# Kernel optimization log

Measured on AMD Instinct MI355X. Metric: run time of the kernel, lower is better.

## Reference

```python
import jax, jax.numpy as jnp
import numpy as np

N_FEAT = 6
EMBED = 256
PAIRS = N_FEAT * (N_FEAT - 1) // 2  # 15
B, S = 32, 512


def setup_inputs() -> dict:
    key = jax.random.key(0)
    k1, k2, k3, k4, k5, k6 = jax.random.split(key, 6)
    features = jax.random.normal(k1, (N_FEAT, B, S, EMBED), dtype=jnp.float32)
    W_pair = jax.random.normal(k2, (PAIRS, 2 * EMBED, EMBED), dtype=jnp.float32) * 0.05
    b_pair = jax.random.normal(k3, (PAIRS, EMBED), dtype=jnp.float32) * 0.05
    W_final = jax.random.normal(k4, (PAIRS * EMBED, EMBED), dtype=jnp.float32) * 0.02
    b_final = jax.random.normal(k5, (EMBED,), dtype=jnp.float32) * 0.02
    NAS = jax.random.randint(k6, (N_FEAT,), 0, 2, dtype=jnp.int32)
    return {"features": features, "W_pair": W_pair, "b_pair": b_pair,
            "W_final": W_final, "b_final": b_final, "NAS": NAS}


def reference(features, W_pair, b_pair, W_final, b_final, NAS):
    n = features.shape[0]
    # static pair index order matches the nested loops: (0,1),(0,2),...,(n-2,n-1)
    i_idx, j_idx = np.triu_indices(n, k=1)
    nas = NAS.at[:2].set(1)  # encoder_input=True forces first two features on
    pair_mask = (nas[i_idx] * nas[j_idx]).astype(features.dtype)  # [P]
    # pairwise concat + linear + tanh, batched over all P pairs
    xcat = jnp.concatenate([features[i_idx], features[j_idx]], axis=-1)  # [P,B,S,2D]
    h = jnp.tanh(jnp.einsum('pbsk,pkd->pbsd', xcat, W_pair) + b_pair[:, None, None, :])
    h = h * pair_mask[:, None, None, None]  # zero out inactive pairs (ZeroNormal)
    P, Bb, Ss, D = h.shape
    # concat along last dim in pair order, then final linear
    flat = jnp.transpose(h, (1, 2, 0, 3)).reshape(Bb, Ss, P * D)  # [B,S,P*D]
    return flat @ W_final + b_final
```

## Files before the change

kernel.cpp:

```cpp
#include <hip/hip_runtime.h>
#include <hip/hip_bf16.h>


typedef unsigned short u16;
typedef __bf16 bf16x8 __attribute__((ext_vector_type(8)));
typedef float f32x4 __attribute__((ext_vector_type(4)));

#define BS 16384
#define EMB 256
#define PAIRS 15
#define XR 264

__constant__ int c_pi[PAIRS] = {0,0,0,0,0,1,1,1,1,2,2,2,3,3,4};
__constant__ int c_pj[PAIRS] = {1,2,3,4,5,2,3,4,5,3,4,5,4,5,5};

__device__ __forceinline__ u16 f2bf_u(float x) {
    __bf16 b = (__bf16)x;
    return __builtin_bit_cast(u16, b);
}

__global__ __launch_bounds__(256) void transpose_cvt2(
    const float* __restrict__ Wp, const float* __restrict__ Wf,
    u16* __restrict__ Wp_t, u16* __restrict__ Wf_t)
{
    __shared__ float t[32][33];
    const int z = blockIdx.z;
    const float* in;
    u16* out;
    int R;
    if (z < PAIRS) { R = 512;  in = Wp + (size_t)z * 512 * 256; out = Wp_t + (size_t)z * 256 * 512; }
    else           { R = 3840; in = Wf;                          out = Wf_t; }
    const int r0 = blockIdx.x * 32;
    if (r0 >= R) return;
    const int c0 = blockIdx.y * 32;
    const int tr = threadIdx.x >> 5;
    const int tc = threadIdx.x & 31;
#pragma unroll
    for (int pass = 0; pass < 4; ++pass)
        t[pass * 8 + tr][tc] = in[(size_t)(r0 + pass * 8 + tr) * 256 + c0 + tc];
    __syncthreads();
#pragma unroll
    for (int pass = 0; pass < 4; ++pass)
        out[(size_t)(c0 + pass * 8 + tr) * R + r0 + tc] = f2bf_u(t[tc][pass * 8 + tr]);
}


__device__ __forceinline__ void stage_tile(const u16* gsrc, int row_stride_us,
                                           int col_off_us, u16* lds_base, int tid) {
    int wave = tid >> 6;
#pragma unroll
    for (int r = 0; r < 2; ++r) {
        int c  = r * 512 + tid;
        int n  = c & 255;
        int kb = c >> 8;
        const u16* g = gsrc + (size_t)n * row_stride_us + col_off_us + kb * 8;
        u16* l = lds_base + (size_t)(r * 512 + wave * 64) * 8;
        __builtin_amdgcn_global_load_lds(
            (const __attribute__((address_space(1))) void*)g,
            (__attribute__((address_space(3))) void*)l,
            16, 0, 0);
    }
}

__device__ __forceinline__ void xpanel_load(const float* fsrc, int t0,
                                            int xrow, int xcg, f32x4* xb) {
#pragma unroll
    for (int i = 0; i < 8; ++i)
        xb[i] = __builtin_nontemporal_load(
            (const f32x4*)(fsrc + (size_t)(t0 + xrow) * EMB + i * 32 + xcg));
}

__device__ __forceinline__ void xpanel_write(const f32x4* xb, u16* ldsx,
                                             int xrow, int xcg) {
#pragma unroll
    for (int i = 0; i < 8; ++i) {
        ushort4 o;
        o.x = f2bf_u(xb[i][0]); o.y = f2bf_u(xb[i][1]);
        o.z = f2bf_u(xb[i][2]); o.w = f2bf_u(xb[i][3]);
        *(ushort4*)(&ldsx[xrow * XR + i * 32 + xcg]) = o;
    }
}

__global__ __launch_bounds__(512, 2) void fused_cblock(
    const float* __restrict__ feats,
    const u16* __restrict__ Wp_t,
    const float* __restrict__ b_pair,
    const u16* __restrict__ Wf_t,
    const float* __restrict__ b_final,
    const int* __restrict__ NAS,
    float* __restrict__ out)
{
    __shared__ u16 lds_b[2][8192];
    __shared__ u16 lds_xA[64 * XR];
    __shared__ u16 lds_xB[64 * XR];
    __shared__ u16 lds_h[64 * XR];

    const int tid  = threadIdx.x;
    const int lane = tid & 63;
    const int wave = tid >> 6;
    const int wm   = wave & 1;
    const int wn   = wave >> 1;
    const int quad = lane >> 4;
    const int l16  = lane & 15;
    const int t0   = blockIdx.x * 64;
    const int xrow = tid >> 3;
    const int xcg  = (tid & 7) * 4;

    int nasv[6];
#pragma unroll
    for (int f = 0; f < 6; ++f) nasv[f] = (f < 2) ? 1 : (NAS[f] != 0 ? 1 : 0);
    int pmask = 0;
#pragma unroll
    for (int p = 0; p < PAIRS; ++p)
        if (nasv[c_pi[p]] & nasv[c_pj[p]]) pmask |= (1 << p);

    f32x4 xb[8];
    xpanel_load(feats, t0, xrow, xcg, xb);
    stage_tile(Wp_t, 512, 0, lds_b[0], tid);
    xpanel_write(xb, lds_xA, xrow, xcg);
    __syncthreads();

    const f32x4 fzero = {0.f, 0.f, 0.f, 0.f};
    f32x4 acc2[8];
#pragma unroll
    for (int i = 0; i < 8; ++i) acc2[i] = fzero;

    for (int p = 0; p < PAIRS; ++p) {
        if (!((pmask >> p) & 1)) continue;
        const int fj = c_pj[p];
        const u16* WpT = Wp_t + (size_t)p * 256 * 512;
        const int rest  = pmask >> (p + 1);
        const int pnext = rest ? (p + 1 + __builtin_ctz(rest)) : -1;

        f32x4 acc1[8];
#pragma unroll
        for (int i = 0; i < 8; ++i) acc1[i] = fzero;

        for (int ks = 0; ks < 16; ++ks) {
            const int cur = ks & 1;
            if (ks == 0)
                xpanel_load(feats + (size_t)fj * BS * EMB, t0, xrow, xcg, xb);
            if (ks < 15)
                stage_tile(WpT, 512, (ks + 1) * 32, lds_b[1 - cur], tid);
            else
                stage_tile(Wf_t, 3840, p * 256, lds_b[1 - cur], tid);
            const u16* xs = (ks < 8) ? lds_xA : lds_xB;
            const int ko = (ks & 7) * 32 + quad * 8;
            bf16x8 a0 = *(const bf16x8*)(&xs[(wm * 32 + l16) * XR + ko]);
            bf16x8 a1 = *(const bf16x8*)(&xs[(wm * 32 + 16 + l16) * XR + ko]);
#pragma unroll
            for (int nt = 0; nt < 4; ++nt) {
                const int n = wn * 64 + nt * 16 + l16;
                bf16x8 b = *(const bf16x8*)(&lds_b[cur][(quad * 256 + n) * 8]);
                acc1[nt]     = __builtin_amdgcn_mfma_f32_16x16x32_bf16(a0, b, acc1[nt],     0, 0, 0);
                acc1[4 + nt] = __builtin_amdgcn_mfma_f32_16x16x32_bf16(a1, b, acc1[4 + nt], 0, 0, 0);
            }
            if (ks == 7)
                xpanel_write(xb, lds_xB, xrow, xcg);
            __syncthreads();
        }

#pragma unroll
        for (int mt = 0; mt < 2; ++mt)
#pragma unroll
        for (int nt = 0; nt < 4; ++nt) {
            const int n = wn * 64 + nt * 16 + l16;
            const float bias = b_pair[p * 256 + n];
#pragma unroll
            for (int r = 0; r < 4; ++r) {
                const int row = wm * 32 + mt * 16 + quad * 4 + r;
                lds_h[row * XR + n] = f2bf_u(tanhf(acc1[mt * 4 + nt][r] + bias));
            }
        }
        __syncthreads();

        for (int ks = 0; ks < 8; ++ks) {
            const int cur = ks & 1;
            if (ks == 0 && pnext >= 0)
                xpanel_load(feats + (size_t)c_pi[pnext] * BS * EMB, t0, xrow, xcg, xb);
            if (ks < 7)
                stage_tile(Wf_t, 3840, p * 256 + (ks + 1) * 32, lds_b[1 - cur], tid);
            else
                stage_tile(Wp_t + (size_t)((pnext >= 0) ? pnext : p) * 256 * 512,
                           512, 0, lds_b[1 - cur], tid);
            const int e0 = ks * 32 + quad * 8;
            bf16x8 a0 = *(const bf16x8*)(&lds_h[(wm * 32 + l16) * XR + e0]);
            bf16x8 a1 = *(const bf16x8*)(&lds_h[(wm * 32 + 16 + l16) * XR + e0]);
#pragma unroll
            for (int nt = 0; nt < 4; ++nt) {
                const int n = wn * 64 + nt * 16 + l16;
                bf16x8 b = *(const bf16x8*)(&lds_b[cur][(quad * 256 + n) * 8]);
                acc2[nt]     = __builtin_amdgcn_mfma_f32_16x16x32_bf16(a0, b, acc2[nt],     0, 0, 0);
                acc2[4 + nt] = __builtin_amdgcn_mfma_f32_16x16x32_bf16(a1, b, acc2[4 + nt], 0, 0, 0);
            }
            if (ks == 7 && pnext >= 0)
                xpanel_write(xb, lds_xA, xrow, xcg);
            __syncthreads();
        }
    }

#pragma unroll
    for (int mt = 0; mt < 2; ++mt)
#pragma unroll
    for (int nt = 0; nt < 4; ++nt) {
        const int n = wn * 64 + nt * 16 + l16;
        const float bf = b_final[n];
#pragma unroll
        for (int r = 0; r < 4; ++r) {
            const int t = t0 + wm * 32 + mt * 16 + quad * 4 + r;
            __builtin_nontemporal_store(acc2[mt * 4 + nt][r] + bf,
                                        &out[(size_t)t * EMB + n]);
        }
    }
}


#define TOK 4

__global__ __launch_bounds__(256) void fallback_cblock(
    const float* __restrict__ feats, const float* __restrict__ W_pair,
    const float* __restrict__ b_pair, const float* __restrict__ W_final,
    const float* __restrict__ b_final, const int* __restrict__ NAS,
    float* __restrict__ out)
{
    __shared__ float xs[TOK][6 * 256];
    __shared__ float hf[TOK][PAIRS * 256];

    const int n  = threadIdx.x;
    const int t0 = blockIdx.x * TOK;

#pragma unroll
    for (int tk = 0; tk < TOK; ++tk)
#pragma unroll
        for (int f = 0; f < 6; ++f)
            xs[tk][f * 256 + n] = feats[((size_t)f * BS + t0 + tk) * EMB + n];
    __syncthreads();

    int nasv[6];
#pragma unroll
    for (int f = 0; f < 6; ++f) nasv[f] = (f < 2) ? 1 : (NAS[f] != 0 ? 1 : 0);

    for (int p = 0; p < PAIRS; ++p) {
        const int fi = c_pi[p], fj = c_pj[p];
        if (!(nasv[fi] & nasv[fj])) {
#pragma unroll
            for (int tk = 0; tk < TOK; ++tk) hf[tk][p * 256 + n] = 0.f;
            continue;
        }
        float acc[TOK];
        const float bias = b_pair[p * 256 + n];
#pragma unroll
        for (int tk = 0; tk < TOK; ++tk) acc[tk] = bias;
        const float* Wp = W_pair + (size_t)p * 512 * 256;
#pragma unroll 4
        for (int k = 0; k < 512; ++k) {
            const float w = Wp[(size_t)k * 256 + n];
            const int xoff = ((k < 256) ? fi : fj) * 256 + (k & 255);
#pragma unroll
            for (int tk = 0; tk < TOK; ++tk) acc[tk] += xs[tk][xoff] * w;
        }
#pragma unroll
        for (int tk = 0; tk < TOK; ++tk)
            hf[tk][p * 256 + n] = tanhf(acc[tk]);
    }
    __syncthreads();

    float acc[TOK];
    const float bf = b_final[n];
#pragma unroll
    for (int tk = 0; tk < TOK; ++tk) acc[tk] = bf;
#pragma unroll 4
    for (int k = 0; k < PAIRS * 256; ++k) {
        const float w = W_final[(size_t)k * 256 + n];
#pragma unroll
        for (int tk = 0; tk < TOK; ++tk) acc[tk] += hf[tk][k] * w;
    }
#pragma unroll
    for (int tk = 0; tk < TOK; ++tk)
        out[(size_t)(t0 + tk) * EMB + n] = acc[tk];
}


extern "C" void kernel_launch(void* const* d_in, const int* in_sizes, int n_in,
                              void* d_out, int out_size, void* d_ws, size_t ws_size,
                              hipStream_t stream) {
    const float* feats   = (const float*)d_in[0];
    const float* W_pair  = (const float*)d_in[1];
    const float* b_pair  = (const float*)d_in[2];
    const float* W_final = (const float*)d_in[3];
    const float* b_final = (const float*)d_in[4];
    const int*   NAS     = (const int*)d_in[5];

    const size_t needed = ((size_t)PAIRS * 256 * 512 + (size_t)256 * 3840) * 2;

    if (ws_size >= needed) {
        u16* Wp_t = (u16*)d_ws;
        u16* Wf_t = Wp_t + (size_t)PAIRS * 256 * 512;
        transpose_cvt2<<<dim3(3840 / 32, 256 / 32, PAIRS + 1), 256, 0, stream>>>(
            W_pair, W_final, Wp_t, Wf_t);
        fused_cblock<<<BS / 64, 512, 0, stream>>>(feats, Wp_t, b_pair, Wf_t,
                                                  b_final, NAS, (float*)d_out);
    } else {
        fallback_cblock<<<BS / TOK, 256, 0, stream>>>(feats, W_pair, b_pair,
                                                      W_final, b_final, NAS,
                                                      (float*)d_out);
    }
}
```

Baseline: 176.5 us.

## Triple-buffer weight tiles with prefetch distance two and one barrier per step

```diff
diff --git a/kernel.cpp b/kernel.cpp
--- a/kernel.cpp
+++ b/kernel.cpp
@@ -81,6 +81,18 @@
     }
 }
 
+__device__ __forceinline__ void phase_barrier() {
+    asm volatile("s_waitcnt vmcnt(2) lgkmcnt(0)" ::: "memory");
+    __builtin_amdgcn_sched_barrier(0);
+    __builtin_amdgcn_s_barrier();
+    __builtin_amdgcn_sched_barrier(0);
+}
+
+__device__ __forceinline__ void full_drain() {
+    asm volatile("s_waitcnt vmcnt(0)" ::: "memory");
+    __builtin_amdgcn_sched_barrier(0);
+}
+
 __global__ __launch_bounds__(512, 2) void fused_cblock(
     const float* __restrict__ feats,
     const u16* __restrict__ Wp_t,
@@ -90,7 +102,7 @@
     const int* __restrict__ NAS,
     float* __restrict__ out)
 {
-    __shared__ u16 lds_b[2][8192];
+    __shared__ u16 lds_b[3][8192];
     __shared__ u16 lds_xA[64 * XR];
     __shared__ u16 lds_xB[64 * XR];
     __shared__ u16 lds_h[64 * XR];
@@ -116,14 +128,16 @@
 
     f32x4 xb[8];
     xpanel_load(feats, t0, xrow, xcg, xb);
-    stage_tile(Wp_t, 512, 0, lds_b[0], tid);
     xpanel_write(xb, lds_xA, xrow, xcg);
-    __syncthreads();
+    stage_tile(Wp_t, 512, 0,  lds_b[0], tid);
+    stage_tile(Wp_t, 512, 32, lds_b[1], tid);
 
     const f32x4 fzero = {0.f, 0.f, 0.f, 0.f};
     f32x4 acc2[8];
 #pragma unroll
     for (int i = 0; i < 8; ++i) acc2[i] = fzero;
+
+    int bcur = 0, bw = 2;
 
     for (int p = 0; p < PAIRS; ++p) {
         if (!((pmask >> p) & 1)) continue;
@@ -135,15 +149,19 @@
         f32x4 acc1[8];
 #pragma unroll
         for (int i = 0; i < 8; ++i) acc1[i] = fzero;
+        float breg[4];
 
         for (int ks = 0; ks < 16; ++ks) {
-            const int cur = ks & 1;
-            if (ks == 0)
-                xpanel_load(feats + (size_t)fj * BS * EMB, t0, xrow, xcg, xb);
-            if (ks < 15)
-                stage_tile(WpT, 512, (ks + 1) * 32, lds_b[1 - cur], tid);
-            else
-                stage_tile(Wf_t, 3840, p * 256, lds_b[1 - cur], tid);
+            phase_barrier();
+            {
+                const u16* gp; int rs, co;
+                const int idx = ks + 2;
+                if (idx <= 15)      { gp = WpT;  rs = 512;  co = idx * 32; }
+                else if (idx == 16) { gp = Wf_t; rs = 3840; co = p * 256; }
+                else                { gp = Wf_t; rs = 3840; co = p * 256 + 32; }
+                stage_tile(gp, rs, co, lds_b[bw], tid);
+            }
+            __builtin_amdgcn_sched_barrier(0);
             const u16* xs = (ks < 8) ? lds_xA : lds_xB;
             const int ko = (ks & 7) * 32 + quad * 8;
             bf16x8 a0 = *(const bf16x8*)(&xs[(wm * 32 + l16) * XR + ko]);
@@ -151,13 +169,21 @@
 #pragma unroll
             for (int nt = 0; nt < 4; ++nt) {
                 const int n = wn * 64 + nt * 16 + l16;
-                bf16x8 b = *(const bf16x8*)(&lds_b[cur][(quad * 256 + n) * 8]);
+                bf16x8 b = *(const bf16x8*)(&lds_b[bcur][(quad * 256 + n) * 8]);
                 acc1[nt]     = __builtin_amdgcn_mfma_f32_16x16x32_bf16(a0, b, acc1[nt],     0, 0, 0);
                 acc1[4 + nt] = __builtin_amdgcn_mfma_f32_16x16x32_bf16(a1, b, acc1[4 + nt], 0, 0, 0);
             }
-            if (ks == 7)
+            if (ks == 7) {
+                __builtin_amdgcn_sched_barrier(0);
+#pragma unroll
+                for (int nt = 0; nt < 4; ++nt)
+                    breg[nt] = b_pair[p * 256 + wn * 64 + nt * 16 + l16];
+                xpanel_load(feats + (size_t)fj * BS * EMB, t0, xrow, xcg, xb);
+                full_drain();
                 xpanel_write(xb, lds_xB, xrow, xcg);
-            __syncthreads();
+            }
+            bcur = (bcur == 2) ? 0 : bcur + 1;
+            bw   = (bw   == 2) ? 0 : bw   + 1;
         }
 
 #pragma unroll
@@ -165,39 +191,48 @@
 #pragma unroll
         for (int nt = 0; nt < 4; ++nt) {
             const int n = wn * 64 + nt * 16 + l16;
-            const float bias = b_pair[p * 256 + n];
 #pragma unroll
             for (int r = 0; r < 4; ++r) {
                 const int row = wm * 32 + mt * 16 + quad * 4 + r;
-                lds_h[row * XR + n] = f2bf_u(tanhf(acc1[mt * 4 + nt][r] + bias));
-            }
-        }
-        __syncthreads();
+                lds_h[row * XR + n] = f2bf_u(tanhf(acc1[mt * 4 + nt][r] + breg[nt]));
+            }
+        }
 
         for (int ks = 0; ks < 8; ++ks) {
-            const int cur = ks & 1;
-            if (ks == 0 && pnext >= 0)
-                xpanel_load(feats + (size_t)c_pi[pnext] * BS * EMB, t0, xrow, xcg, xb);
-            if (ks < 7)
-                stage_tile(Wf_t, 3840, p * 256 + (ks + 1) * 32, lds_b[1 - cur], tid);
-            else
-                stage_tile(Wp_t + (size_t)((pnext >= 0) ? pnext : p) * 256 * 512,
-                           512, 0, lds_b[1 - cur], tid);
+            phase_barrier();
+            {
+                const u16* gp; int rs, co;
+                const int idx = ks + 2;
+                if (idx <= 7) { gp = Wf_t; rs = 3840; co = p * 256 + idx * 32; }
+                else {
+                    const int np = (pnext >= 0) ? pnext : p;
+                    gp = Wp_t + (size_t)np * 256 * 512; rs = 512; co = (idx - 8) * 32;
+                }
+                stage_tile(gp, rs, co, lds_b[bw], tid);
+            }
+            __builtin_amdgcn_sched_barrier(0);
             const int e0 = ks * 32 + quad * 8;
             bf16x8 a0 = *(const bf16x8*)(&lds_h[(wm * 32 + l16) * XR + e0]);
             bf16x8 a1 = *(const bf16x8*)(&lds_h[(wm * 32 + 16 + l16) * XR + e0]);
 #pragma unroll
             for (int nt = 0; nt < 4; ++nt) {
                 const int n = wn * 64 + nt * 16 + l16;
-                bf16x8 b = *(const bf16x8*)(&lds_b[cur][(quad * 256 + n) * 8]);
+                bf16x8 b = *(const bf16x8*)(&lds_b[bcur][(quad * 256 + n) * 8]);
                 acc2[nt]     = __builtin_amdgcn_mfma_f32_16x16x32_bf16(a0, b, acc2[nt],     0, 0, 0);
                 acc2[4 + nt] = __builtin_amdgcn_mfma_f32_16x16x32_bf16(a1, b, acc2[4 + nt], 0, 0, 0);
             }
-            if (ks == 7 && pnext >= 0)
+            if (ks == 7 && pnext >= 0) {
+                __builtin_amdgcn_sched_barrier(0);
+                xpanel_load(feats + (size_t)c_pi[pnext] * BS * EMB, t0, xrow, xcg, xb);
+                full_drain();
                 xpanel_write(xb, lds_xA, xrow, xcg);
-            __syncthreads();
-        }
-    }
+            }
+            bcur = (bcur == 2) ? 0 : bcur + 1;
+            bw   = (bw   == 2) ? 0 : bw   + 1;
+        }
+    }
+
+    asm volatile("s_waitcnt vmcnt(0)" ::: "memory");
 
 #pragma unroll
     for (int mt = 0; mt < 2; ++mt)
```

After: 180.3 us. +2.2%, slower.
